# Optimization experiments

Measured on AMD Instinct MI355X. Metric: run time of the kernel, lower is better.

The kernel has to match this reference:

```python
import jax, jax.numpy as jnp
import numpy as np

# Each of the 16 two-input logic ops op_i(a,b) is linear in {1, a, b, a*b}:
# op_i = c0 + ca*a + cb*b + cab*a*b. Rows follow the standard difflogic order:
# 0, a&b, a&~b, a, ~a&b, b, a^b, a|b, ~(a|b), ~(a^b), ~b, a|~b, ~a, ~a|b, ~(a&b), 1
OP_COEFFS = np.array([
    [0.0, 0.0, 0.0, 0.0],
    [0.0, 0.0, 0.0, 1.0],
    [0.0, 1.0, 0.0, -1.0],
    [0.0, 1.0, 0.0, 0.0],
    [0.0, 0.0, 1.0, -1.0],
    [0.0, 0.0, 1.0, 0.0],
    [0.0, 1.0, 1.0, -2.0],
    [0.0, 1.0, 1.0, -1.0],
    [1.0, -1.0, -1.0, 1.0],
    [1.0, -1.0, -1.0, 2.0],
    [1.0, 0.0, -1.0, 0.0],
    [1.0, 0.0, -1.0, 1.0],
    [1.0, -1.0, 0.0, 0.0],
    [1.0, -1.0, 0.0, 1.0],
    [1.0, 0.0, 0.0, -1.0],
    [1.0, 0.0, 0.0, 0.0],
], dtype=np.float32)

STRIDE_H, STRIDE_W = 1, 1
PAD_H, PAD_W = 1, 1
KERNEL_H, KERNEL_W = 3, 3


def setup_inputs() -> dict:
    key = jax.random.key(0)
    k1, k2 = jax.random.split(key, 2)
    N, C_in, H, W = 32, 64, 32, 32
    C_out = 512
    x = jax.random.uniform(k1, (N, C_in, H, W), dtype=jnp.float32)
    weights = jax.random.normal(k2, (C_out, 4, 16), dtype=jnp.float32)
    # selection packs (channel << 16) | (row_offset << 8) | col_offset per the
    # module's unpack_selection; offsets live inside the 3x3 kernel window.
    rng = np.random.default_rng(0)
    ch = rng.integers(0, C_in, (C_out, 8))
    ry = rng.integers(0, KERNEL_H, (C_out, 8))
    rx = rng.integers(0, KERNEL_W, (C_out, 8))
    selection = jnp.asarray((ch << 16) | (ry << 8) | rx, dtype=jnp.int32)
    return {"x": x, "weights": weights, "selection": selection}


def reference(x, weights, selection):
    N, C_in, H, W = x.shape
    C_out = selection.shape[0]
    H_out = (H + 2 * PAD_H - KERNEL_H) // STRIDE_H + 1
    W_out = (W + 2 * PAD_W - KERNEL_W) // STRIDE_W + 1
    # zero-pad: out-of-bounds gathers read 0.0 in the original implementation
    xp = jnp.pad(x, ((0, 0), (0, 0), (PAD_H, PAD_H), (PAD_W, PAD_W)))
    ch = (selection >> 16) & 0xFFFF   # [C_out, 8]
    ry = (selection >> 8) & 0xFF
    rx = selection & 0xFF
    oy = jnp.arange(H_out)
    ox = jnp.arange(W_out)
    rows = oy[None, :, None] * STRIDE_H + ry[:, None, :]   # [C_out, H_out, 8]
    cols = ox[None, :, None] * STRIDE_W + rx[:, None, :]   # [C_out, W_out, 8]
    # gather: g[n,c,oy,ox,k] = xp[n, ch[c,k], rows[c,oy,k], cols[c,ox,k]]
    g = xp[:, ch[:, None, None, :], rows[:, :, None, :], cols[:, None, :, :]]  # [N,C_out,H_out,W_out,8]
    a = g[..., 0::2]   # [N, C_out, H_out, W_out, 4]
    b = g[..., 1::2]
    # training path: softmax over the 16 logic functions, then fold the 16 ops
    # into linear coefficients over {1, a, b, a*b} (exact same math as bin_op_s)
    w_prob = jax.nn.softmax(weights, axis=-1)                      # [C_out, 4, 16]
    coef = jnp.einsum('cpi,ij->cpj', w_prob, jnp.asarray(OP_COEFFS))  # [C_out, 4, 4]
    k0 = coef[None, :, None, None, :, 0]
    ka = coef[None, :, None, None, :, 1]
    kb = coef[None, :, None, None, :, 2]
    kab = coef[None, :, None, None, :, 3]
    y = k0 + ka * a + kb * b + kab * (a * b)   # [N, C_out, H_out, W_out, 4]
    return y
```

## Files before the change

### kernel.cpp

```cpp
#include <hip/hip_runtime.h>

#define N_BATCH 32
#define C_IN    64
#define H_IN    32
#define W_IN    32
#define C_OUT   512
#define H_OUT   32
#define W_OUT   32

typedef float f32x4 __attribute__((ext_vector_type(4)));

__device__ __forceinline__ void op_coeffs(int i, float& c0, float& c1, float& c2, float& c3) {
    constexpr float T[16][4] = {
        {0.f,0.f,0.f,0.f}, {0.f,0.f,0.f,1.f}, {0.f,1.f,0.f,-1.f}, {0.f,1.f,0.f,0.f},
        {0.f,0.f,1.f,-1.f}, {0.f,0.f,1.f,0.f}, {0.f,1.f,1.f,-2.f}, {0.f,1.f,1.f,-1.f},
        {1.f,-1.f,-1.f,1.f}, {1.f,-1.f,-1.f,2.f}, {1.f,0.f,-1.f,0.f}, {1.f,0.f,-1.f,1.f},
        {1.f,-1.f,0.f,0.f}, {1.f,-1.f,0.f,1.f}, {1.f,0.f,0.f,-1.f}, {1.f,0.f,0.f,0.f}
    };
    c0 = T[i][0]; c1 = T[i][1]; c2 = T[i][2]; c3 = T[i][3];
}

__global__ __launch_bounds__(256)
void coef_kernel(const float* __restrict__ weights, f32x4* __restrict__ coef) {
    const int idx = blockIdx.x * 256 + threadIdx.x;
    if (idx >= C_OUT * 4) return;
    const float* w = weights + idx * 16;
    float v[16];
    float m = -3.402823466e+38f;
    #pragma unroll
    for (int i = 0; i < 16; ++i) { v[i] = w[i]; m = fmaxf(m, v[i]); }
    float ssum = 0.f;
    #pragma unroll
    for (int i = 0; i < 16; ++i) { v[i] = __expf(v[i] - m); ssum += v[i]; }
    const float inv = 1.0f / ssum;
    float c0 = 0.f, c1 = 0.f, c2 = 0.f, c3 = 0.f;
    #pragma unroll
    for (int i = 0; i < 16; ++i) {
        float t0, t1, t2, t3;
        op_coeffs(i, t0, t1, t2, t3);
        c0 = fmaf(v[i], t0, c0);
        c1 = fmaf(v[i], t1, c1);
        c2 = fmaf(v[i], t2, c2);
        c3 = fmaf(v[i], t3, c3);
    }
    f32x4 out; out.x = c0 * inv; out.y = c1 * inv; out.z = c2 * inv; out.w = c3 * inv;
    coef[idx] = out;
}

__device__ __forceinline__ float gather_x(const float* __restrict__ x,
                                          int nbase, int s, int oh, int ow) {
    int ch = (s >> 16) & 0xffff;
    int ry = (s >> 8) & 0xff;
    int rx = s & 0xff;
    int r = oh + ry - 1;
    int c = ow + rx - 1;
    bool ok = ((unsigned)r < (unsigned)H_IN) && ((unsigned)c < (unsigned)W_IN);
    return ok ? x[nbase + ch * (H_IN * W_IN) + r * W_IN + c] : 0.0f;
}

__global__ __launch_bounds__(256)
void conv_main_kernel(const float* __restrict__ x,
                      const f32x4* __restrict__ coef,
                      const int*   __restrict__ sel,
                      float* __restrict__ y) {
    const int c = blockIdx.x;
    const int n = blockIdx.y;

    const int sl0 = sel[c * 8 + 0], sl1 = sel[c * 8 + 1];
    const int sl2 = sel[c * 8 + 2], sl3 = sel[c * 8 + 3];
    const int sl4 = sel[c * 8 + 4], sl5 = sel[c * 8 + 5];
    const int sl6 = sel[c * 8 + 6], sl7 = sel[c * 8 + 7];
    const f32x4 cf0 = coef[c * 4 + 0];
    const f32x4 cf1 = coef[c * 4 + 1];
    const f32x4 cf2 = coef[c * 4 + 2];
    const f32x4 cf3 = coef[c * 4 + 3];

    const int nbase = n * (C_IN * H_IN * W_IN);
    f32x4* __restrict__ yv = reinterpret_cast<f32x4*>(y) +
                             (size_t)(n * C_OUT + c) * (H_OUT * W_OUT);

    #pragma unroll
    for (int k = 0; k < 4; ++k) {
        const int pos = threadIdx.x + k * 256;
        const int oh = pos >> 5;
        const int ow = pos & 31;

        float a, b;
        f32x4 out;

        a = gather_x(x, nbase, sl0, oh, ow);
        b = gather_x(x, nbase, sl1, oh, ow);
        out.x = fmaf(cf0.w * a, b, fmaf(cf0.y, a, fmaf(cf0.z, b, cf0.x)));

        a = gather_x(x, nbase, sl2, oh, ow);
        b = gather_x(x, nbase, sl3, oh, ow);
        out.y = fmaf(cf1.w * a, b, fmaf(cf1.y, a, fmaf(cf1.z, b, cf1.x)));

        a = gather_x(x, nbase, sl4, oh, ow);
        b = gather_x(x, nbase, sl5, oh, ow);
        out.z = fmaf(cf2.w * a, b, fmaf(cf2.y, a, fmaf(cf2.z, b, cf2.x)));

        a = gather_x(x, nbase, sl6, oh, ow);
        b = gather_x(x, nbase, sl7, oh, ow);
        out.w = fmaf(cf3.w * a, b, fmaf(cf3.y, a, fmaf(cf3.z, b, cf3.x)));

        __builtin_nontemporal_store(out, &yv[pos]);
    }
}

__global__ __launch_bounds__(256)
void conv_fused_kernel(const float* __restrict__ x,
                       const float* __restrict__ weights,
                       const int*   __restrict__ sel,
                       float* __restrict__ y) {
    const int c = blockIdx.x;
    const int n = blockIdx.y;

    __shared__ float4 s_coef[4];
    __shared__ int    s_sel[8];

    if (threadIdx.x < 8) s_sel[threadIdx.x] = sel[c * 8 + threadIdx.x];
    if (threadIdx.x < 4) {
        const int p = threadIdx.x;
        const float* w = weights + (c * 4 + p) * 16;
        float v[16];
        float m = -3.402823466e+38f;
        #pragma unroll
        for (int i = 0; i < 16; ++i) { v[i] = w[i]; m = fmaxf(m, v[i]); }
        float ssum = 0.f;
        #pragma unroll
        for (int i = 0; i < 16; ++i) { v[i] = __expf(v[i] - m); ssum += v[i]; }
        const float inv = 1.0f / ssum;
        float c0 = 0.f, c1 = 0.f, c2 = 0.f, c3 = 0.f;
        #pragma unroll
        for (int i = 0; i < 16; ++i) {
            float t0, t1, t2, t3;
            op_coeffs(i, t0, t1, t2, t3);
            c0 = fmaf(v[i], t0, c0);
            c1 = fmaf(v[i], t1, c1);
            c2 = fmaf(v[i], t2, c2);
            c3 = fmaf(v[i], t3, c3);
        }
        s_coef[p] = make_float4(c0 * inv, c1 * inv, c2 * inv, c3 * inv);
    }
    __syncthreads();

    const int nbase = n * (C_IN * H_IN * W_IN);
    f32x4* __restrict__ yv = reinterpret_cast<f32x4*>(y) +
                             (size_t)(n * C_OUT + c) * (H_OUT * W_OUT);

    const float4 cf0 = s_coef[0], cf1 = s_coef[1], cf2 = s_coef[2], cf3 = s_coef[3];
    const int sl0 = s_sel[0], sl1 = s_sel[1], sl2 = s_sel[2], sl3 = s_sel[3];
    const int sl4 = s_sel[4], sl5 = s_sel[5], sl6 = s_sel[6], sl7 = s_sel[7];

    #pragma unroll
    for (int k = 0; k < 4; ++k) {
        const int pos = threadIdx.x + k * 256;
        const int oh = pos >> 5;
        const int ow = pos & 31;
        float a, b;
        f32x4 out;
        a = gather_x(x, nbase, sl0, oh, ow);
        b = gather_x(x, nbase, sl1, oh, ow);
        out.x = fmaf(cf0.w * a, b, fmaf(cf0.y, a, fmaf(cf0.z, b, cf0.x)));
        a = gather_x(x, nbase, sl2, oh, ow);
        b = gather_x(x, nbase, sl3, oh, ow);
        out.y = fmaf(cf1.w * a, b, fmaf(cf1.y, a, fmaf(cf1.z, b, cf1.x)));
        a = gather_x(x, nbase, sl4, oh, ow);
        b = gather_x(x, nbase, sl5, oh, ow);
        out.z = fmaf(cf2.w * a, b, fmaf(cf2.y, a, fmaf(cf2.z, b, cf2.x)));
        a = gather_x(x, nbase, sl6, oh, ow);
        b = gather_x(x, nbase, sl7, oh, ow);
        out.w = fmaf(cf3.w * a, b, fmaf(cf3.y, a, fmaf(cf3.z, b, cf3.x)));
        __builtin_nontemporal_store(out, &yv[pos]);
    }
}

extern "C" void kernel_launch(void* const* d_in, const int* in_sizes, int n_in,
                              void* d_out, int out_size, void* d_ws, size_t ws_size,
                              hipStream_t stream) {
    const float* x       = (const float*)d_in[0];
    const float* weights = (const float*)d_in[1];
    const int*   sel     = (const int*)d_in[2];
    float* y             = (float*)d_out;

    const size_t coef_bytes = (size_t)C_OUT * 4 * sizeof(f32x4);
    dim3 grid(C_OUT, N_BATCH);

    if (ws_size >= coef_bytes) {
        f32x4* coef = (f32x4*)d_ws;
        coef_kernel<<<dim3((C_OUT * 4 + 255) / 256), 256, 0, stream>>>(weights, coef);
        conv_main_kernel<<<grid, 256, 0, stream>>>(x, coef, sel, y);
    } else {
        conv_fused_kernel<<<grid, 256, 0, stream>>>(x, weights, sel, y);
    }
}
```

Baseline: 56.96 us.

## Pre-pad input into workspace and drop bounds checks from gather loop

```diff
diff --git a/kernel.cpp b/kernel.cpp
--- a/kernel.cpp
+++ b/kernel.cpp
@@ -7,6 +7,9 @@
 #define C_OUT   512
 #define H_OUT   32
 #define W_OUT   32
+
+#define PH      34
+#define PSTRIDE (PH * PH)
 
 typedef float f32x4 __attribute__((ext_vector_type(4)));
 
@@ -21,30 +24,101 @@
 }
 
 __global__ __launch_bounds__(256)
-void coef_kernel(const float* __restrict__ weights, f32x4* __restrict__ coef) {
-    const int idx = blockIdx.x * 256 + threadIdx.x;
-    if (idx >= C_OUT * 4) return;
-    const float* w = weights + idx * 16;
-    float v[16];
-    float m = -3.402823466e+38f;
+void prep_kernel(const float* __restrict__ x,
+                 const float* __restrict__ weights,
+                 f32x4* __restrict__ coef,
+                 float* __restrict__ xpad) {
+    const int blk = blockIdx.x;
+    if (blk < 8) {
+        const int idx = blk * 256 + threadIdx.x;
+        const float* w = weights + idx * 16;
+        float v[16];
+        float m = -3.402823466e+38f;
+        #pragma unroll
+        for (int i = 0; i < 16; ++i) { v[i] = w[i]; m = fmaxf(m, v[i]); }
+        float ssum = 0.f;
+        #pragma unroll
+        for (int i = 0; i < 16; ++i) { v[i] = __expf(v[i] - m); ssum += v[i]; }
+        const float inv = 1.0f / ssum;
+        float c0 = 0.f, c1 = 0.f, c2 = 0.f, c3 = 0.f;
+        #pragma unroll
+        for (int i = 0; i < 16; ++i) {
+            float t0, t1, t2, t3;
+            op_coeffs(i, t0, t1, t2, t3);
+            c0 = fmaf(v[i], t0, c0);
+            c1 = fmaf(v[i], t1, c1);
+            c2 = fmaf(v[i], t2, c2);
+            c3 = fmaf(v[i], t3, c3);
+        }
+        f32x4 out; out.x = c0 * inv; out.y = c1 * inv; out.z = c2 * inv; out.w = c3 * inv;
+        coef[idx] = out;
+    } else {
+        const int p = blk - 8;
+        const float* __restrict__ src = x    + (size_t)p * (H_IN * W_IN);
+        float*       __restrict__ dst = xpad + (size_t)p * PSTRIDE;
+        for (int e = threadIdx.x; e < PSTRIDE; e += 256) {
+            const int r  = e / PH;
+            const int cc = e - r * PH;
+            const unsigned ri = (unsigned)(r - 1), ci = (unsigned)(cc - 1);
+            float v = (ri < W_IN && ci < W_IN) ? src[ri * W_IN + ci] : 0.0f;
+            dst[e] = v;
+        }
+    }
+}
+
+__global__ __launch_bounds__(256)
+void conv_main_padded(const float* __restrict__ xpad,
+                      const f32x4* __restrict__ coef,
+                      const int*   __restrict__ sel,
+                      float* __restrict__ y) {
+    const int c = blockIdx.x;
+    const int n = blockIdx.y;
+
+    const int s0 = sel[c * 8 + 0], s1 = sel[c * 8 + 1];
+    const int s2 = sel[c * 8 + 2], s3 = sel[c * 8 + 3];
+    const int s4 = sel[c * 8 + 4], s5 = sel[c * 8 + 5];
+    const int s6 = sel[c * 8 + 6], s7 = sel[c * 8 + 7];
+    const f32x4 cf0 = coef[c * 4 + 0];
+    const f32x4 cf1 = coef[c * 4 + 1];
+    const f32x4 cf2 = coef[c * 4 + 2];
+    const f32x4 cf3 = coef[c * 4 + 3];
+
+    const float* __restrict__ pb = xpad + (size_t)n * (C_IN * PSTRIDE);
+    #define PLANE(s) (pb + ((s) >> 16) * PSTRIDE + (((s) >> 8) & 0xff) * PH + ((s) & 0xff))
+    const float* __restrict__ p0 = PLANE(s0);
+    const float* __restrict__ p1 = PLANE(s1);
+    const float* __restrict__ p2 = PLANE(s2);
+    const float* __restrict__ p3 = PLANE(s3);
+    const float* __restrict__ p4 = PLANE(s4);
+    const float* __restrict__ p5 = PLANE(s5);
+    const float* __restrict__ p6 = PLANE(s6);
+    const float* __restrict__ p7 = PLANE(s7);
+    #undef PLANE
+
+    f32x4* __restrict__ yv = reinterpret_cast<f32x4*>(y) +
+                             (size_t)(n * C_OUT + c) * (H_OUT * W_OUT);
+
+    int pos  = threadIdx.x;
+    int poff = (pos >> 5) * PH + (pos & 31);
+
     #pragma unroll
-    for (int i = 0; i < 16; ++i) { v[i] = w[i]; m = fmaxf(m, v[i]); }
-    float ssum = 0.f;
-    #pragma unroll
-    for (int i = 0; i < 16; ++i) { v[i] = __expf(v[i] - m); ssum += v[i]; }
-    const float inv = 1.0f / ssum;
-    float c0 = 0.f, c1 = 0.f, c2 = 0.f, c3 = 0.f;
-    #pragma unroll
-    for (int i = 0; i < 16; ++i) {
-        float t0, t1, t2, t3;
-        op_coeffs(i, t0, t1, t2, t3);
-        c0 = fmaf(v[i], t0, c0);
-        c1 = fmaf(v[i], t1, c1);
-        c2 = fmaf(v[i], t2, c2);
-        c3 = fmaf(v[i], t3, c3);
-    }
-    f32x4 out; out.x = c0 * inv; out.y = c1 * inv; out.z = c2 * inv; out.w = c3 * inv;
-    coef[idx] = out;
+    for (int k = 0; k < 4; ++k) {
+        const float a0 = p0[poff], b0 = p1[poff];
+        const float a1 = p2[poff], b1 = p3[poff];
+        const float a2 = p4[poff], b2 = p5[poff];
+        const float a3 = p6[poff], b3 = p7[poff];
+
+        f32x4 out;
+        out.x = fmaf(cf0.w * a0, b0, fmaf(cf0.y, a0, fmaf(cf0.z, b0, cf0.x)));
+        out.y = fmaf(cf1.w * a1, b1, fmaf(cf1.y, a1, fmaf(cf1.z, b1, cf1.x)));
+        out.z = fmaf(cf2.w * a2, b2, fmaf(cf2.y, a2, fmaf(cf2.z, b2, cf2.x)));
+        out.w = fmaf(cf3.w * a3, b3, fmaf(cf3.y, a3, fmaf(cf3.z, b3, cf3.x)));
+
+        __builtin_nontemporal_store(out, &yv[pos]);
+
+        pos  += 256;
+        poff += 8 * PH;
+    }
 }
 
 __device__ __forceinline__ float gather_x(const float* __restrict__ x,
@@ -56,56 +130,6 @@
     int c = ow + rx - 1;
     bool ok = ((unsigned)r < (unsigned)H_IN) && ((unsigned)c < (unsigned)W_IN);
     return ok ? x[nbase + ch * (H_IN * W_IN) + r * W_IN + c] : 0.0f;
-}
-
-__global__ __launch_bounds__(256)
-void conv_main_kernel(const float* __restrict__ x,
-                      const f32x4* __restrict__ coef,
-                      const int*   __restrict__ sel,
-                      float* __restrict__ y) {
-    const int c = blockIdx.x;
-    const int n = blockIdx.y;
-
-    const int sl0 = sel[c * 8 + 0], sl1 = sel[c * 8 + 1];
-    const int sl2 = sel[c * 8 + 2], sl3 = sel[c * 8 + 3];
-    const int sl4 = sel[c * 8 + 4], sl5 = sel[c * 8 + 5];
-    const int sl6 = sel[c * 8 + 6], sl7 = sel[c * 8 + 7];
-    const f32x4 cf0 = coef[c * 4 + 0];
-    const f32x4 cf1 = coef[c * 4 + 1];
-    const f32x4 cf2 = coef[c * 4 + 2];
-    const f32x4 cf3 = coef[c * 4 + 3];
-
-    const int nbase = n * (C_IN * H_IN * W_IN);
-    f32x4* __restrict__ yv = reinterpret_cast<f32x4*>(y) +
-                             (size_t)(n * C_OUT + c) * (H_OUT * W_OUT);
-
-    #pragma unroll
-    for (int k = 0; k < 4; ++k) {
-        const int pos = threadIdx.x + k * 256;
-        const int oh = pos >> 5;
-        const int ow = pos & 31;
-
-        float a, b;
-        f32x4 out;
-
-        a = gather_x(x, nbase, sl0, oh, ow);
-        b = gather_x(x, nbase, sl1, oh, ow);
-        out.x = fmaf(cf0.w * a, b, fmaf(cf0.y, a, fmaf(cf0.z, b, cf0.x)));
-
-        a = gather_x(x, nbase, sl2, oh, ow);
-        b = gather_x(x, nbase, sl3, oh, ow);
-        out.y = fmaf(cf1.w * a, b, fmaf(cf1.y, a, fmaf(cf1.z, b, cf1.x)));
-
-        a = gather_x(x, nbase, sl4, oh, ow);
-        b = gather_x(x, nbase, sl5, oh, ow);
-        out.z = fmaf(cf2.w * a, b, fmaf(cf2.y, a, fmaf(cf2.z, b, cf2.x)));
-
-        a = gather_x(x, nbase, sl6, oh, ow);
-        b = gather_x(x, nbase, sl7, oh, ow);
-        out.w = fmaf(cf3.w * a, b, fmaf(cf3.y, a, fmaf(cf3.z, b, cf3.x)));
-
-        __builtin_nontemporal_store(out, &yv[pos]);
-    }
 }
 
 __global__ __launch_bounds__(256)
@@ -185,12 +209,14 @@
     float* y             = (float*)d_out;
 
     const size_t coef_bytes = (size_t)C_OUT * 4 * sizeof(f32x4);
+    const size_t pad_bytes  = (size_t)N_BATCH * C_IN * PSTRIDE * sizeof(float);
     dim3 grid(C_OUT, N_BATCH);
 
-    if (ws_size >= coef_bytes) {
+    if (ws_size >= coef_bytes + pad_bytes) {
         f32x4* coef = (f32x4*)d_ws;
-        coef_kernel<<<dim3((C_OUT * 4 + 255) / 256), 256, 0, stream>>>(weights, coef);
-        conv_main_kernel<<<grid, 256, 0, stream>>>(x, coef, sel, y);
+        float* xpad = (float*)((char*)d_ws + coef_bytes);
+        prep_kernel<<<dim3(8 + N_BATCH * C_IN), 256, 0, stream>>>(x, weights, coef, xpad);
+        conv_main_padded<<<grid, 256, 0, stream>>>(xpad, coef, sel, y);
     } else {
         conv_fused_kernel<<<grid, 256, 0, stream>>>(x, weights, sel, y);
     }
```

Result: slower. 59.21 us (+4.0%).
